# Optimization experiments

Measured on AMD Instinct MI355X. Metric: run time of the kernel, lower is better.

## Reference

```python
import jax, jax.numpy as jnp
import numpy as np

N = 10000      # nodes
E = 160000     # edges
MUL = 64       # multiplicity of 0e and 1o in node feats / target
NATTR = 10     # number of element types (node_attrs one-hot width)
RDIM = 8       # radial (edge_feats) dim
NAVG = 16.0    # num_avg_neighbors
_INV3 = 0.5773502691896258  # CG coeff for 1o x 1o -> 0e (1/sqrt(3))


def setup_inputs() -> dict:
    key = jax.random.key(0)
    ks = jax.random.split(key, 20)
    return {
        "node_attrs": jax.random.uniform(ks[0], (N, NATTR), jnp.float32),
        "node_feats": jax.random.normal(ks[1], (N, 4 * MUL), jnp.float32),
        "edge_attrs_real": jax.random.normal(ks[2], (E, 4), jnp.float32),
        "edge_attrs_imag": jax.random.normal(ks[3], (E, 4), jnp.float32),
        "edge_feats": jax.random.normal(ks[4], (E, RDIM), jnp.float32),
        # linear_up (per-l internal weights)
        "W_up0": jax.random.normal(ks[5], (MUL, MUL), jnp.float32),
        "W_up1": jax.random.normal(ks[6], (MUL, MUL), jnp.float32),
        # conv_tp_weights MLP: [8, 64, 64, 64, 4*MUL]
        "M1": jax.random.normal(ks[7], (RDIM, 64), jnp.float32),
        "M2": jax.random.normal(ks[8], (64, 64), jnp.float32),
        "M3": jax.random.normal(ks[9], (64, 64), jnp.float32),
        "M4": jax.random.normal(ks[10], (64, 4 * MUL), jnp.float32),
        # linear: irreps_mid (128x0e+128x1o) -> irreps_nonlin (128x0e+64x1o)
        "W_lin_s": jax.random.normal(ks[11], (2 * MUL, 2 * MUL), jnp.float32),
        "W_lin_v": jax.random.normal(ks[12], (2 * MUL, MUL), jnp.float32),
        # skip_tp: FullyConnectedTensorProduct(node_feats, node_attrs -> irreps_nonlin)
        "W_sk_s": jax.random.normal(ks[13], (MUL, NATTR, 2 * MUL), jnp.float32),
        "W_sk_v": jax.random.normal(ks[14], (MUL, NATTR, MUL), jnp.float32),
        "edge_index": jax.random.randint(ks[15], (2, E), 0, N, jnp.int64
                                         if jax.config.jax_enable_x64 else jnp.int32),
    }


def _forward(node_attrs, node_feats, edge_attrs_real, edge_attrs_imag, edge_feats,
             W_up0, W_up1, M1, M2, M3, M4, W_lin_s, W_lin_v, W_sk_s, W_sk_v,
             sender, receiver):
    n = node_feats.shape[0]
    x0 = node_feats[:, :MUL]                          # (N, 64)   64x0e
    x1 = node_feats[:, MUL:].reshape(n, MUL, 3)       # (N, 64, 3) 64x1o

    # skip TP (fully connected, node_attrs are scalars)
    sk_norm = 1.0 / np.sqrt(MUL * NATTR)
    sc_s = jnp.einsum('nu,na,uav->nv', x0, node_attrs, W_sk_s) * sk_norm   # (N,128)
    sc_v = jnp.einsum('nui,na,uav->nvi', x1, node_attrs, W_sk_v) * sk_norm # (N,64,3)

    # linear_up (per-l)
    up_norm = 1.0 / np.sqrt(MUL)
    x0 = (x0 @ W_up0) * up_norm
    x1 = jnp.einsum('nui,uv->nvi', x1, W_up1) * up_norm

    # radial MLP -> per-edge TP weights (4 uvu paths x MUL)
    h = jax.nn.silu((edge_feats @ M1) / np.sqrt(RDIM))
    h = jax.nn.silu((h @ M2) / 8.0)
    h = jax.nn.silu((h @ M3) / 8.0)
    tw = (h @ M4) / 8.0                               # (E, 256)
    wA, wB, wC, wD = (tw[:, :MUL], tw[:, MUL:2*MUL],
                      tw[:, 2*MUL:3*MUL], tw[:, 3*MUL:])

    xs0 = x0[sender]                                  # (E, 64)
    xs1 = x1[sender]                                  # (E, 64, 3)

    def conv_tp(y):
        # y: (E,4) = [0e | 1o]; uvu paths with per-edge weights
        y0, y1 = y[:, :1], y[:, 1:]
        s = jnp.concatenate([xs0 * y0 * wA,                                  # 0e x 0e -> 0e
                             jnp.einsum('eui,ei->eu', xs1, y1) * _INV3 * wD  # 1o x 1o -> 0e
                             ], axis=1)                                      # (E,128)
        v = jnp.concatenate([(xs0 * wB)[:, :, None] * y1[:, None, :],        # 0e x 1o -> 1o
                             xs1 * (y0 * wC)[:, :, None]                     # 1o x 0e -> 1o
                             ], axis=1)                                      # (E,128,3)
        return s, v

    sr, vr = conv_tp(edge_attrs_real)
    si, vi = conv_tp(edge_attrs_imag)

    ms_r = jax.ops.segment_sum(sr, receiver, num_segments=n)
    mv_r = jax.ops.segment_sum(vr, receiver, num_segments=n)
    ms_i = jax.ops.segment_sum(si, receiver, num_segments=n)
    mv_i = jax.ops.segment_sum(vi, receiver, num_segments=n)

    lin_norm = (1.0 / np.sqrt(2 * MUL)) / (2.0 * NAVG)

    def lin(ms, mv):
        return (ms @ W_lin_s) * lin_norm, jnp.einsum('nui,uv->nvi', mv, W_lin_v) * lin_norm

    def gate(s, v):
        # irreps_nonlin = 64x0e scalars | 64x0e gates | 64x1o gated
        scal = jax.nn.silu(s[:, :MUL])
        g = jax.nn.silu(s[:, MUL:])
        return jnp.concatenate([scal, (v * g[:, :, None]).reshape(n, 3 * MUL)], axis=1)

    ls, lv = lin(ms_r, mv_r)
    real = gate(ls + sc_s, lv + sc_v)                 # (N, 256), residual on real part
    lsi, lvi = lin(ms_i, mv_i)
    imag = gate(lsi, lvi)                             # (N, 256)

    # view_as_complex + reshape [N, num_features, dim//num_features]; complex kept
    # as trailing real/imag axis of size 2.
    return jnp.stack([real, imag], axis=-1).reshape(n, MUL, (4 * MUL) // MUL, 2)


def reference(node_attrs, node_feats, edge_attrs_real, edge_attrs_imag, edge_feats,
              W_up0, W_up1, M1, M2, M3, M4, W_lin_s, W_lin_v, W_sk_s, W_sk_v,
              edge_index):
    sender, receiver = edge_index[0], edge_index[1]
    return _forward(node_attrs, node_feats, edge_attrs_real, edge_attrs_imag,
                    edge_feats, W_up0, W_up1, M1, M2, M3, M4,
                    W_lin_s, W_lin_v, W_sk_s, W_sk_v, sender, receiver)
```

## Files before the change

### kernel.cpp

```cpp
#include <hip/hip_runtime.h>
#include <hip/hip_bf16.h>

#define NN 10000
#define NE 160000
#define NGRP 625
#define XPLN 640000

#define SK_NORM   0.039528470752104741f
#define UP_NORM   0.125f
#define M1_NORM   0.35355339059327373f
#define INV3      0.5773502691896258f
#define LIN_NORM  0.0027621358640099516f

__device__ __forceinline__ float siluf(float x) { return x / (1.0f + __expf(-x)); }

__device__ __forceinline__ unsigned short f2bf_bits(float x) {
    union { __hip_bfloat16 h; unsigned short u; } cv;
    cv.h = __float2bfloat16(x);
    return cv.u;
}
__device__ __forceinline__ float bflo(unsigned int w) { return __uint_as_float(w << 16); }
__device__ __forceinline__ float bfhi(unsigned int w) { return __uint_as_float(w & 0xffff0000u); }

typedef short bf16x8 __attribute__((ext_vector_type(8)));
typedef float f32x4  __attribute__((ext_vector_type(4)));

__global__ __launch_bounds__(256) void k_detect(const int* __restrict__ ei32, int* __restrict__ flag) {
    __shared__ int cnt;
    if (threadIdx.x == 0) cnt = 0;
    __syncthreads();
    int z = 0;
    for (int i = threadIdx.x; i < 1024; i += 256)
        if (ei32[2 * i + 1] == 0) z++;
    atomicAdd(&cnt, z);
    __syncthreads();
    if (threadIdx.x == 0) flag[0] = (cnt >= 512) ? 1 : 0;
}

__global__ __launch_bounds__(256) void k_cvt(const int* __restrict__ ei32, const int* __restrict__ flag,
                                             int* __restrict__ snd, int* __restrict__ rcv) {
    int e = blockIdx.x * 256 + threadIdx.x;
    if (e >= NE) return;
    if (flag[0]) {
        const long long* e64 = (const long long*)ei32;
        snd[e] = (int)e64[e];
        rcv[e] = (int)e64[NE + e];
    } else {
        snd[e] = ei32[e];
        rcv[e] = ei32[NE + e];
    }
}

__global__ __launch_bounds__(256) void k_wprepN(
    const float* __restrict__ Wsk_s, const float* __restrict__ Wsk_v,
    const float* __restrict__ Wu0, const float* __restrict__ Wu1,
    unsigned short* __restrict__ WNF) {
    int idx = blockIdx.x * 256 + threadIdx.x;
    if (idx >= 131072) return;
    float val;
    if (idx < 81920) {
        int p = idx / 10240, r = idx % 10240;
        int kc = r >> 9, l8 = r & 511;
        int lane = l8 >> 3, j = l8 & 7, quad = lane >> 4, lo = lane & 15;
        int a = kc >> 1, u = (kc & 1) * 32 + quad * 8 + j;
        val = Wsk_s[(u * 10 + a) * 128 + p * 16 + lo];
    } else if (idx < 122880) {
        int rel = idx - 81920;
        int p = rel / 10240, r = rel % 10240;
        int kc = r >> 9, l8 = r & 511;
        int lane = l8 >> 3, j = l8 & 7, quad = lane >> 4, lo = lane & 15;
        int a = kc >> 1, u = (kc & 1) * 32 + quad * 8 + j;
        val = Wsk_v[(u * 10 + a) * 64 + p * 16 + lo];
    } else if (idx < 126976) {
        int rel = idx - 122880;
        int p = rel >> 10, r = rel & 1023;
        int kc = r >> 9, l8 = r & 511;
        int lane = l8 >> 3, j = l8 & 7, quad = lane >> 4, lo = lane & 15;
        int u = kc * 32 + quad * 8 + j;
        val = Wu0[u * 64 + p * 16 + lo];
    } else {
        int rel = idx - 126976;
        int p = rel >> 10, r = rel & 1023;
        int kc = r >> 9, l8 = r & 511;
        int lane = l8 >> 3, j = l8 & 7, quad = lane >> 4, lo = lane & 15;
        int u = kc * 32 + quad * 8 + j;
        val = Wu1[u * 64 + p * 16 + lo];
    }
    WNF[idx] = f2bf_bits(val);
}

__global__ __launch_bounds__(256) void k_xprep(
    const float* __restrict__ node_attrs, const float* __restrict__ node_feats,
    unsigned short* __restrict__ xpk, float* __restrict__ attrsP) {
    int idx = blockIdx.x * 256 + threadIdx.x;
    if (idx < 4 * NN * 64) {
        int n = idx >> 8, c = idx & 255;
        int plane = c >> 6, u = c & 63;
        float v = (plane == 0) ? node_feats[(long)n * 256 + u]
                               : node_feats[(long)n * 256 + 64 + u * 3 + (plane - 1)];
        xpk[(size_t)plane * XPLN + (long)n * 64 + u] = f2bf_bits(v);
        return;
    }
    int i2 = idx - 4 * NN * 64;
    if (i2 < 10 * NN) {
        int a = i2 / NN, n = i2 - a * NN;
        attrsP[i2] = node_attrs[(long)n * 10 + a];
    }
}

__global__ __launch_bounds__(256) void k_wprep2(
    const float* __restrict__ M1, const float* __restrict__ M2,
    const float* __restrict__ M3, const float* __restrict__ M4,
    const float* __restrict__ W_lin_s, const float* __restrict__ W_lin_v,
    unsigned short* __restrict__ WFG, unsigned short* __restrict__ WLF) {
    int idx = blockIdx.x * 256 + threadIdx.x;
    if (idx >= (52 + 48) * 512) return;
    if (idx < 52 * 512) {
        int f = idx >> 9, r = idx & 511;
        int lane = r >> 3, j = r & 7;
        int quad = lane >> 4, lo = lane & 15;
        float val;
        if (f < 4) {
            int n = f * 16 + lo, k = quad * 8 + j;
            val = (k < 8) ? M1[k * 64 + n] : 0.f;
        } else if (f < 12) {
            int g2 = f - 4, nt = g2 >> 1, half = g2 & 1;
            int n = nt * 16 + lo, k = half * 32 + quad * 8 + j;
            val = M2[k * 64 + n];
        } else if (f < 20) {
            int g3 = f - 12, nt = g3 >> 1, half = g3 & 1;
            int n = nt * 16 + lo, k = half * 32 + quad * 8 + j;
            val = M3[k * 64 + n];
        } else {
            int g4 = f - 20, tt = g4 >> 1, half = g4 & 1;
            int n = tt * 16 + lo, k = half * 32 + quad * 8 + j;
            val = M4[k * 256 + n];
        }
        WFG[idx] = f2bf_bits(val);
    } else {
        int rel = idx - 52 * 512;
        int f = rel >> 9, r = rel & 511;
        int lane = r >> 3, j = r & 7;
        int quad = lane >> 4, lo = lane & 15;
        float val;
        if (f < 32) {
            int vt = f >> 2, ks = f & 3;
            val = W_lin_s[(ks * 32 + quad * 8 + j) * 128 + vt * 16 + lo];
        } else {
            int f2 = f - 32;
            int vt = f2 >> 2, ks = f2 & 3;
            val = W_lin_v[(ks * 32 + quad * 8 + j) * 64 + vt * 16 + lo];
        }
        WLF[rel] = f2bf_bits(val);
    }
}

#define G0 8
#define NB0 79
#define G2 4
#define NB2 157
#define G3 16
#define NB3 40
#define KNODE_GRID (4*NB0 + 2*NB2 + 2*NB3)

__global__ __launch_bounds__(128) void k_node(
    const unsigned short* __restrict__ xpk, const float* __restrict__ attrsP,
    const unsigned short* __restrict__ WNF,
    float* __restrict__ sc_s, float* __restrict__ sc_v,
    float* __restrict__ x0u, float* __restrict__ x1p) {
    __shared__ unsigned short pan[2 * 10240];
    __shared__ float att[10 * 128];

    int t = threadIdx.x;
    int bid = blockIdx.x;
    int type, vp, chunk;
    if (bid < 4 * NB0)                 { type = 0; vp = bid / NB0; chunk = bid % NB0; }
    else if (bid < 4 * NB0 + 2 * NB2)  { int r = bid - 4 * NB0; type = 2; vp = r / NB2; chunk = r % NB2; }
    else                               { int r = bid - 4 * NB0 - 2 * NB2; type = 3; vp = r / NB3; chunk = r % NB3; }
    int G = (type == 0) ? G0 : (type == 2 ? G2 : G3);
    int g0 = chunk * G;
    int ng = NGRP - g0; if (ng > G) ng = G;
    int n0 = g0 * 16;

    int psrc, pcnt;
    if (type == 0)      { psrc = vp * 2 * 10240;           pcnt = 20480; }
    else if (type == 2) { psrc = 81920 + vp * 2 * 10240;   pcnt = 20480; }
    else                { psrc = 122880 + vp * 2 * 1024;   pcnt = 2048;  }
    for (int i = t; i < pcnt / 8; i += 128)
        ((float4*)pan)[i] = ((const float4*)(WNF + psrc))[i];
    if (type == 3) {
        for (int i = t; i < 2048 / 8; i += 128)
            ((float4*)(pan + 2048))[i] = ((const float4*)(WNF + 126976 + vp * 2 * 1024))[i];
    }
    if (type <= 2) {
        int cnt = ng * 16;
        #pragma unroll
        for (int k = 0; k < 10; k++) {
            int i = k * 128 + t;
            int nl = t;
            if (nl < cnt) att[i] = attrsP[k * NN + n0 + nl];
        }
    }
    __syncthreads();

    int wv = t >> 6, lane = t & 63, lo = lane & 15, quad = lane >> 4;
    int lbase = lane * 8;
    const f32x4 zacc = {0.f, 0.f, 0.f, 0.f};
    const unsigned short* mypan = pan + wv * 10240;

    if (type == 0) {
        int vtg = vp * 2 + wv;
        const unsigned short* xb = xpk;
        bf16x8 nfa0 = *(const bf16x8*)(xb + (long)(n0 + lo) * 64 + quad * 8);
        bf16x8 nfa1 = *(const bf16x8*)(xb + (long)(n0 + lo) * 64 + 32 + quad * 8);
        #pragma unroll 1
        for (int g = 0; g < ng; g++) {
            bf16x8 fa0 = nfa0, fa1 = nfa1;
            if (g + 1 < ng) {
                nfa0 = *(const bf16x8*)(xb + (long)(n0 + (g + 1) * 16 + lo) * 64 + quad * 8);
                nfa1 = *(const bf16x8*)(xb + (long)(n0 + (g + 1) * 16 + lo) * 64 + 32 + quad * 8);
            }
            f32x4 acc = zacc;
            #pragma unroll
            for (int a = 0; a < 10; a++) {
                bf16x8 b0 = *(const bf16x8*)&mypan[(2 * a) * 512 + lbase];
                bf16x8 b1 = *(const bf16x8*)&mypan[(2 * a + 1) * 512 + lbase];
                f32x4 p = __builtin_amdgcn_mfma_f32_16x16x32_bf16(fa0, b0, zacc, 0, 0, 0);
                p = __builtin_amdgcn_mfma_f32_16x16x32_bf16(fa1, b1, p, 0, 0, 0);
                float4 afv = *(const float4*)&att[a * 128 + g * 16 + quad * 4];
                acc[0] += afv.x * p[0]; acc[1] += afv.y * p[1];
                acc[2] += afv.z * p[2]; acc[3] += afv.w * p[3];
            }
            int nb = n0 + g * 16;
            #pragma unroll
            for (int r = 0; r < 4; r++)
                sc_s[(long)(nb + quad * 4 + r) * 128 + vtg * 16 + lo] = acc[r] * SK_NORM;
        }
    } else if (type == 2) {
        int vt = vp * 2 + wv;
        bf16x8 nfa0[3], nfa1[3];
        #pragma unroll
        for (int i = 0; i < 3; i++) {
            const unsigned short* xb = xpk + (size_t)(1 + i) * XPLN + (long)(n0 + lo) * 64;
            nfa0[i] = *(const bf16x8*)(xb + quad * 8);
            nfa1[i] = *(const bf16x8*)(xb + 32 + quad * 8);
        }
        #pragma unroll 1
        for (int g = 0; g < ng; g++) {
            bf16x8 fa0[3], fa1[3];
            #pragma unroll
            for (int i = 0; i < 3; i++) { fa0[i] = nfa0[i]; fa1[i] = nfa1[i]; }
            if (g + 1 < ng) {
                #pragma unroll
                for (int i = 0; i < 3; i++) {
                    const unsigned short* xb = xpk + (size_t)(1 + i) * XPLN + (long)(n0 + (g + 1) * 16 + lo) * 64;
                    nfa0[i] = *(const bf16x8*)(xb + quad * 8);
                    nfa1[i] = *(const bf16x8*)(xb + 32 + quad * 8);
                }
            }
            f32x4 acc0 = zacc, acc1 = zacc, acc2 = zacc;
            #pragma unroll
            for (int a = 0; a < 10; a++) {
                bf16x8 b0 = *(const bf16x8*)&mypan[(2 * a) * 512 + lbase];
                bf16x8 b1 = *(const bf16x8*)&mypan[(2 * a + 1) * 512 + lbase];
                float4 afv = *(const float4*)&att[a * 128 + g * 16 + quad * 4];
                f32x4 p0 = __builtin_amdgcn_mfma_f32_16x16x32_bf16(fa0[0], b0, zacc, 0, 0, 0);
                p0 = __builtin_amdgcn_mfma_f32_16x16x32_bf16(fa1[0], b1, p0, 0, 0, 0);
                acc0[0] += afv.x * p0[0]; acc0[1] += afv.y * p0[1];
                acc0[2] += afv.z * p0[2]; acc0[3] += afv.w * p0[3];
                f32x4 p1 = __builtin_amdgcn_mfma_f32_16x16x32_bf16(fa0[1], b0, zacc, 0, 0, 0);
                p1 = __builtin_amdgcn_mfma_f32_16x16x32_bf16(fa1[1], b1, p1, 0, 0, 0);
                acc1[0] += afv.x * p1[0]; acc1[1] += afv.y * p1[1];
                acc1[2] += afv.z * p1[2]; acc1[3] += afv.w * p1[3];
                f32x4 p2 = __builtin_amdgcn_mfma_f32_16x16x32_bf16(fa0[2], b0, zacc, 0, 0, 0);
                p2 = __builtin_amdgcn_mfma_f32_16x16x32_bf16(fa1[2], b1, p2, 0, 0, 0);
                acc2[0] += afv.x * p2[0]; acc2[1] += afv.y * p2[1];
                acc2[2] += afv.z * p2[2]; acc2[3] += afv.w * p2[3];
            }
            int nb = n0 + g * 16;
            #pragma unroll
            for (int r = 0; r < 4; r++) {
                long rb = (long)(nb + quad * 4 + r) * 192 + vt * 16 + lo;
                sc_v[rb]       = acc0[r] * SK_NORM;
                sc_v[rb + 64]  = acc1[r] * SK_NORM;
                sc_v[rb + 128] = acc2[r] * SK_NORM;
            }
        }
    } else {
        int vt = vp * 2 + wv;
        bf16x8 bk20 = *(const bf16x8*)&pan[wv * 1024 + lbase];
        bf16x8 bk21 = *(const bf16x8*)&pan[wv * 1024 + 512 + lbase];
        bf16x8 bk30 = *(const bf16x8*)&pan[2048 + wv * 1024 + lbase];
        bf16x8 bk31 = *(const bf16x8*)&pan[2048 + wv * 1024 + 512 + lbase];
        #pragma unroll 1
        for (int g = 0; g < ng; g++) {
            int nb = n0 + g * 16;
            {
                const unsigned short* xb = xpk + (long)(nb + lo) * 64;
                bf16x8 fa0 = *(const bf16x8*)(xb + quad * 8);
                bf16x8 fa1 = *(const bf16x8*)(xb + 32 + quad * 8);
                f32x4 acc = __builtin_amdgcn_mfma_f32_16x16x32_bf16(fa0, bk20, zacc, 0, 0, 0);
                acc = __builtin_amdgcn_mfma_f32_16x16x32_bf16(fa1, bk21, acc, 0, 0, 0);
                #pragma unroll
                for (int r = 0; r < 4; r++)
                    x0u[(long)(nb + quad * 4 + r) * 64 + vt * 16 + lo] = acc[r] * UP_NORM;
            }
            #pragma unroll
            for (int i = 0; i < 3; i++) {
                const unsigned short* xb = xpk + (size_t)(1 + i) * XPLN + (long)(nb + lo) * 64;
                bf16x8 fa0 = *(const bf16x8*)(xb + quad * 8);
                bf16x8 fa1 = *(const bf16x8*)(xb + 32 + quad * 8);
                f32x4 acc = __builtin_amdgcn_mfma_f32_16x16x32_bf16(fa0, bk30, zacc, 0, 0, 0);
                acc = __builtin_amdgcn_mfma_f32_16x16x32_bf16(fa1, bk31, acc, 0, 0, 0);
                #pragma unroll
                for (int r = 0; r < 4; r++)
                    x1p[(size_t)i * XPLN + (long)(nb + quad * 4 + r) * 64 + vt * 16 + lo] = acc[r] * UP_NORM;
            }
        }
    }
}

__global__ __launch_bounds__(256) void k_hist(const int* __restrict__ rcv, int* __restrict__ counts) {
    int e = blockIdx.x * 256 + threadIdx.x;
    if (e < NE) atomicAdd(&counts[rcv[e]], 1);
}

__global__ __launch_bounds__(1024) void k_scan(const int* __restrict__ counts, int* __restrict__ offsets) {
    __shared__ int partial[1024];
    int t = threadIdx.x;
    const int CHUNK = (NN + 1023) / 1024;
    int base = t * CHUNK;
    int s = 0;
    for (int i = 0; i < CHUNK; i++) if (base + i < NN) s += counts[base + i];
    partial[t] = s;
    __syncthreads();
    for (int d = 1; d < 1024; d *= 2) {
        int v = (t >= d) ? partial[t - d] : 0;
        __syncthreads();
        partial[t] += v;
        __syncthreads();
    }
    int excl = (t == 0) ? 0 : partial[t - 1];
    for (int i = 0; i < CHUNK; i++) {
        if (base + i < NN) { offsets[base + i] = excl; excl += counts[base + i]; }
    }
    if (t == 1023) offsets[NN] = partial[1023];
}

__global__ __launch_bounds__(256) void k_fill(const int* __restrict__ rcv, const int* __restrict__ snd,
                                              const int* __restrict__ offsets,
                                              int* __restrict__ cursor, int2* __restrict__ epk) {
    int e = blockIdx.x * 256 + threadIdx.x;
    if (e < NE) {
        int r = rcv[e];
        int pos = atomicAdd(&cursor[r], 1);
        epk[offsets[r] + pos] = make_int2(snd[e], e);
    }
}

__global__ __launch_bounds__(256) void k_eprep(const int2* __restrict__ epk,
                                               const float4* __restrict__ ear, const float4* __restrict__ eai,
                                               const float4* __restrict__ ef,
                                               int* __restrict__ sndp,
                                               float4* __restrict__ earp, float4* __restrict__ eaip,
                                               float4* __restrict__ efp) {
    int j = blockIdx.x * 256 + threadIdx.x;
    if (j >= NE) return;
    int2 se = epk[j];
    sndp[j] = se.x;
    earp[j] = ear[se.y];
    eaip[j] = eai[se.y];
    efp[(long)j * 2]     = ef[(long)se.y * 2];
    efp[(long)j * 2 + 1] = ef[(long)se.y * 2 + 1];
}

#define HID_STRIDE 72
#define OB_STRIDE  40
#define EPB 128

__global__ __launch_bounds__(256) void k_edge_mlp(
    const float4* __restrict__ efp, const unsigned short* __restrict__ WFG,
    __hip_bfloat16* __restrict__ twp) {
    __shared__ unsigned short wfrag[52 * 512];
    __shared__ unsigned short hid[4][16 * HID_STRIDE];

    int t = threadIdx.x;
    for (int i = t; i < 52 * 512 / 8; i += 256)
        ((float4*)wfrag)[i] = ((const float4*)WFG)[i];
    __syncthreads();

    int wv = t >> 6;
    int lane = t & 63;
    int lo = lane & 15;
    int quad = lane >> 4;
    int lbase = lane * 8;
    unsigned short* myhid = hid[wv];
    unsigned short* myob  = hid[wv];
    const f32x4 zacc = {0.f, 0.f, 0.f, 0.f};

    #pragma unroll 1
    for (int g = 0; g < EPB / 64; g++) {
        int jbase = blockIdx.x * EPB + g * 64 + wv * 16;

        bf16x8 a1 = {0, 0, 0, 0, 0, 0, 0, 0};
        if (quad == 0) {
            float4 f0 = efp[(long)(jbase + lo) * 2];
            float4 f1 = efp[(long)(jbase + lo) * 2 + 1];
            union { unsigned short us[8]; bf16x8 v; } pk;
            pk.us[0] = f2bf_bits(f0.x * M1_NORM); pk.us[1] = f2bf_bits(f0.y * M1_NORM);
            pk.us[2] = f2bf_bits(f0.z * M1_NORM); pk.us[3] = f2bf_bits(f0.w * M1_NORM);
            pk.us[4] = f2bf_bits(f1.x * M1_NORM); pk.us[5] = f2bf_bits(f1.y * M1_NORM);
            pk.us[6] = f2bf_bits(f1.z * M1_NORM); pk.us[7] = f2bf_bits(f1.w * M1_NORM);
            a1 = pk.v;
        }
        {
            f32x4 acc[4];
            #pragma unroll
            for (int nt = 0; nt < 4; nt++) {
                bf16x8 b = *(const bf16x8*)&wfrag[nt * 512 + lbase];
                acc[nt] = __builtin_amdgcn_mfma_f32_16x16x32_bf16(a1, b, zacc, 0, 0, 0);
            }
            #pragma unroll
            for (int nt = 0; nt < 4; nt++)
                #pragma unroll
                for (int r = 0; r < 4; r++)
                    myhid[(quad * 4 + r) * HID_STRIDE + nt * 16 + lo] = f2bf_bits(siluf(acc[nt][r]));
        }

        #pragma unroll
        for (int L = 0; L < 2; L++) {
            int fb = 4 + L * 8;
            bf16x8 a0 = *(const bf16x8*)&myhid[lo * HID_STRIDE + quad * 8];
            bf16x8 a1v = *(const bf16x8*)&myhid[lo * HID_STRIDE + 32 + quad * 8];
            f32x4 acc[4];
            #pragma unroll
            for (int nt = 0; nt < 4; nt++) {
                bf16x8 b0 = *(const bf16x8*)&wfrag[(fb + nt * 2) * 512 + lbase];
                bf16x8 b1 = *(const bf16x8*)&wfrag[(fb + nt * 2 + 1) * 512 + lbase];
                acc[nt] = __builtin_amdgcn_mfma_f32_16x16x32_bf16(a0, b0, zacc, 0, 0, 0);
                acc[nt] = __builtin_amdgcn_mfma_f32_16x16x32_bf16(a1v, b1, acc[nt], 0, 0, 0);
            }
            #pragma unroll
            for (int nt = 0; nt < 4; nt++)
                #pragma unroll
                for (int r = 0; r < 4; r++)
                    myhid[(quad * 4 + r) * HID_STRIDE + nt * 16 + lo] = f2bf_bits(siluf(acc[nt][r] * 0.125f));
        }

        {
            bf16x8 a0 = *(const bf16x8*)&myhid[lo * HID_STRIDE + quad * 8];
            bf16x8 a1v = *(const bf16x8*)&myhid[lo * HID_STRIDE + 32 + quad * 8];
            int sedge = lane >> 2, sch = lane & 3;
            #pragma unroll 1
            for (int rd = 0; rd < 8; rd++) {
                f32x4 acc2[2];
                #pragma unroll
                for (int p = 0; p < 2; p++) {
                    int tt = (rd < 4) ? (p * 4 + rd) : (8 + p * 4 + (rd - 4));
                    bf16x8 b0 = *(const bf16x8*)&wfrag[(20 + tt * 2) * 512 + lbase];
                    bf16x8 b1 = *(const bf16x8*)&wfrag[(20 + tt * 2 + 1) * 512 + lbase];
                    acc2[p] = __builtin_amdgcn_mfma_f32_16x16x32_bf16(a0, b0, zacc, 0, 0, 0);
                    acc2[p] = __builtin_amdgcn_mfma_f32_16x16x32_bf16(a1v, b1, acc2[p], 0, 0, 0);
                }
                #pragma unroll
                for (int p = 0; p < 2; p++)
                    #pragma unroll
                    for (int r = 0; r < 4; r++)
                        myob[(quad * 4 + r) * OB_STRIDE + 2 * lo + p] = f2bf_bits(acc2[p][r] * 0.125f);
                bf16x8 vv = *(const bf16x8*)&myob[sedge * OB_STRIDE + sch * 8];
                *(bf16x8*)(twp + (long)(jbase + sedge) * 256 + rd * 32 + sch * 8) = vv;
            }
        }
    }
}

#define CB2 4
__global__ __launch_bounds__(256) void k_conv(
    const int* __restrict__ offsets, const int* __restrict__ sndp,
    const float4* __restrict__ earp, const float4* __restrict__ eaip,
    const float* __restrict__ x0u, const float* __restrict__ x1p,
    const __hip_bfloat16* __restrict__ twp,
    unsigned short* __restrict__ msgF) {
    __shared__ float red[2 * 64 * 9];
    __shared__ unsigned short stg[1024];
    int n = blockIdx.x;
    int t = threadIdx.x;
    int wv = t >> 6;
    int u = t & 63;
    int path = wv >> 1;
    int wpar = wv & 1;
    int beg = offsets[n], end = offsets[n + 1];
    float a0r = 0.f, a1r = 0.f, a2r = 0.f, a3r = 0.f;
    float a0i = 0.f, a1i = 0.f, a2i = 0.f, a3i = 0.f;
    if (path == 0) {
        const int tsel = 2 * u;
        for (int jb = beg + wpar * CB2; jb < end; jb += 2 * CB2) {
            unsigned int twd[CB2]; float x0v[CB2]; float4 yr[CB2], yi[CB2];
            #pragma unroll
            for (int p = 0; p < CB2; p++) {
                int j = jb + p;
                int jc = (j < end) ? j : (end - 1);
                int s = sndp[jc];
                yr[p] = earp[jc];
                yi[p] = eaip[jc];
                x0v[p] = x0u[(long)s * 64 + u];
                twd[p] = (j < end) ? *(const unsigned int*)(twp + (long)jc * 256 + tsel) : 0u;
            }
            #pragma unroll
            for (int p = 0; p < CB2; p++) {
                float wA = bflo(twd[p]), wB = bfhi(twd[p]);
                float xa = x0v[p] * wA, xb = x0v[p] * wB;
                a0r += xa * yr[p].x; a1r += xb * yr[p].y; a2r += xb * yr[p].z; a3r += xb * yr[p].w;
                a0i += xa * yi[p].x; a1i += xb * yi[p].y; a2i += xb * yi[p].z; a3i += xb * yi[p].w;
            }
        }
    } else {
        const int tsel = 128 + 2 * u;
        for (int jb = beg + wpar * CB2; jb < end; jb += 2 * CB2) {
            unsigned int twd[CB2]; float xv0[CB2], xv1[CB2], xv2[CB2]; float4 yr[CB2], yi[CB2];
            #pragma unroll
            for (int p = 0; p < CB2; p++) {
                int j = jb + p;
                int jc = (j < end) ? j : (end - 1);
                int s = sndp[jc];
                yr[p] = earp[jc];
                yi[p] = eaip[jc];
                long sb = (long)s * 64 + u;
                xv0[p] = x1p[sb];
                xv1[p] = x1p[XPLN + sb];
                xv2[p] = x1p[2 * XPLN + sb];
                twd[p] = (j < end) ? *(const unsigned int*)(twp + (long)jc * 256 + tsel) : 0u;
            }
            #pragma unroll
            for (int p = 0; p < CB2; p++) {
                float wC = bflo(twd[p]), wDs = bfhi(twd[p]) * INV3;
                float dr = xv0[p] * yr[p].y + xv1[p] * yr[p].z + xv2[p] * yr[p].w;
                float di = xv0[p] * yi[p].y + xv1[p] * yi[p].z + xv2[p] * yi[p].w;
                a0r += dr * wDs; a0i += di * wDs;
                float ycr = yr[p].x * wC, yci = yi[p].x * wC;
                a1r += xv0[p] * ycr; a2r += xv1[p] * ycr; a3r += xv2[p] * ycr;
                a1i += xv0[p] * yci; a2i += xv1[p] * yci; a3i += xv2[p] * yci;
            }
        }
    }
    float* rb = &red[(path * 64 + u) * 9];
    if (wpar == 1) {
        rb[0] = a0r; rb[1] = a1r; rb[2] = a2r; rb[3] = a3r;
        rb[4] = a0i; rb[5] = a1i; rb[6] = a2i; rb[7] = a3i;
    }
    __syncthreads();
    if (wpar == 0) {
        a0r += rb[0]; a1r += rb[1]; a2r += rb[2]; a3r += rb[3];
        a0i += rb[4]; a1i += rb[5]; a2i += rb[6]; a3i += rb[7];
        int cu = path * 64 + u;
        stg[cu]       = f2bf_bits(a0r);
        stg[128 + cu] = f2bf_bits(a0i);
        stg[256 + cu] = f2bf_bits(a1r);
        stg[384 + cu] = f2bf_bits(a2r);
        stg[512 + cu] = f2bf_bits(a3r);
        stg[640 + cu] = f2bf_bits(a1i);
        stg[768 + cu] = f2bf_bits(a2i);
        stg[896 + cu] = f2bf_bits(a3i);
    }
    __syncthreads();
    if (t < 128) {
        int g = n >> 4, lo = n & 15;
        bf16x8 vv = *(const bf16x8*)&stg[t * 8];
        *(bf16x8*)(msgF + (size_t)g * 16384 + (t >> 2) * 512 + lo * 32 + (t & 3) * 8) = vv;
    }
}

#define SV_STRIDE 129
#define VV_STRIDE 65

__global__ __launch_bounds__(256, 3) void k_lin(
    const unsigned short* __restrict__ msgF,
    const float* __restrict__ sc_s, const float* __restrict__ sc_v,
    const unsigned short* __restrict__ WLF,
    float* __restrict__ out) {
    __shared__ char smem[49152];
    unsigned short* wfrag = (unsigned short*)smem;
    float* sval = (float*)smem;
    float* vval = (float*)(smem + 2 * 16 * SV_STRIDE * 4);

    int t = threadIdx.x;
    for (int i = t; i < 48 * 512 / 8; i += 256)
        ((float4*)wfrag)[i] = ((const float4*)WLF)[i];
    __syncthreads();

    int wv = t >> 6;
    int lane = t & 63;
    int lo = lane & 15;
    int quad = lane >> 4;
    int lbase = lane * 8;
    int aoff_lane = lo * 32 + quad * 8;
    const f32x4 zacc = {0.f, 0.f, 0.f, 0.f};

    long g = blockIdx.x;
    long nbase = g * 16;
    const unsigned short* agbase = msgF + (size_t)g * 16384;

    f32x4 accs[10];
    #pragma unroll
    for (int q = 0; q < 10; q++) {
        int tau = wv + q * 4;
        int cblk, fb;
        if (tau < 16) {
            int ri = tau >> 3, vt = tau & 7;
            cblk = ri; fb = vt * 4;
        } else {
            int tp = tau - 16;
            int ri = tp / 12, rem = tp % 12;
            int i = rem >> 2, vt = rem & 3;
            cblk = 2 + ri * 3 + i; fb = 32 + vt * 4;
        }
        f32x4 acc = zacc;
        #pragma unroll
        for (int ks = 0; ks < 4; ks++) {
            bf16x8 a = *(const bf16x8*)(agbase + (cblk * 4 + ks) * 512 + aoff_lane);
            bf16x8 b = *(const bf16x8*)&wfrag[(fb + ks) * 512 + lbase];
            acc = __builtin_amdgcn_mfma_f32_16x16x32_bf16(a, b, acc, 0, 0, 0);
        }
        accs[q] = acc;
    }
    __syncthreads();

    #pragma unroll
    for (int q = 0; q < 10; q++) {
        int tau = wv + q * 4;
        if (tau < 16) {
            int ri = tau >> 3, vt = tau & 7;
            int cidx = (ri * 16) * SV_STRIDE + vt * 16 + lo;
            #pragma unroll
            for (int r = 0; r < 4; r++)
                sval[cidx + (quad * 4 + r) * SV_STRIDE] = accs[q][r] * LIN_NORM;
        } else {
            int tp = tau - 16;
            int ri = tp / 12, rem = tp % 12;
            int i = rem >> 2, vt = rem & 3;
            int cidx = ((ri * 3 + i) * 16) * VV_STRIDE + vt * 16 + lo;
            #pragma unroll
            for (int r = 0; r < 4; r++)
                vval[cidx + (quad * 4 + r) * VV_STRIDE] = accs[q][r] * LIN_NORM;
        }
    }
    __syncthreads();

    #pragma unroll 1
    for (int j = 0; j < 16; j++) {
        int c = t;
        long gn = nbase + j;
        float re, im;
        if (c < 64) {
            float sr = sval[(0 * 16 + j) * SV_STRIDE + c] + sc_s[gn * 128 + c];
            float si = sval[(1 * 16 + j) * SV_STRIDE + c];
            re = siluf(sr); im = siluf(si);
        } else {
            int rem = c - 64;
            int v = rem / 3;
            int i = rem - v * 3;
            float gr = siluf(sval[(0 * 16 + j) * SV_STRIDE + 64 + v] + sc_s[gn * 128 + 64 + v]);
            float gi = siluf(sval[(1 * 16 + j) * SV_STRIDE + 64 + v]);
            float lr = vval[((0 * 3 + i) * 16 + j) * VV_STRIDE + v] + sc_v[gn * 192 + i * 64 + v];
            float li = vval[((1 * 3 + i) * 16 + j) * VV_STRIDE + v];
            re = lr * gr; im = li * gi;
        }
        ((float2*)out)[gn * 256 + c] = make_float2(re, im);
    }
}

extern "C" void kernel_launch(void* const* d_in, const int* in_sizes, int n_in,
                              void* d_out, int out_size, void* d_ws, size_t ws_size,
                              hipStream_t stream) {
    const float* node_attrs = (const float*)d_in[0];
    const float* node_feats = (const float*)d_in[1];
    const float* ear        = (const float*)d_in[2];
    const float* eai        = (const float*)d_in[3];
    const float* edge_feats = (const float*)d_in[4];
    const float* W_up0      = (const float*)d_in[5];
    const float* W_up1      = (const float*)d_in[6];
    const float* M1         = (const float*)d_in[7];
    const float* M2         = (const float*)d_in[8];
    const float* M3         = (const float*)d_in[9];
    const float* M4         = (const float*)d_in[10];
    const float* W_lin_s    = (const float*)d_in[11];
    const float* W_lin_v    = (const float*)d_in[12];
    const float* W_sk_s     = (const float*)d_in[13];
    const float* W_sk_v     = (const float*)d_in[14];
    const int*   ei         = (const int*)d_in[15];

    char* ws = (char*)d_ws;
    size_t o_x0u = 0;
    size_t o_x1p = o_x0u + (size_t)NN * 64 * 4;
    size_t o_scs = o_x1p + (size_t)NN * 256 * 4;
    size_t o_scv = o_scs + (size_t)NN * 128 * 4;
    size_t o_tw  = o_scv + (size_t)NN * 192 * 4;
    size_t o_cnt = o_tw  + (size_t)NE * 256 * 2;
    size_t o_cur = o_cnt + (size_t)NN * 4;
    size_t o_ofs = o_cur + (size_t)NN * 4;
    size_t o_epk = o_ofs + (size_t)(NN + 1) * 4 + 60;
    size_t o_snd = o_epk + (size_t)NE * 8;
    size_t o_rcv = o_snd + (size_t)NE * 4;
    size_t o_flg = o_rcv + (size_t)NE * 4;
    size_t o_msg = o_flg + 64;
    size_t o_wnf = o_msg + (size_t)NN * 1024 * 2;
    size_t o_snp = o_wnf + 262144;
    size_t o_erp = o_snp + (size_t)NE * 4;
    size_t o_eip = o_erp + (size_t)NE * 16;
    size_t o_efp = o_eip + (size_t)NE * 16;
    size_t o_wfg = o_efp + (size_t)NE * 32;
    size_t o_wlf = o_wfg + (size_t)52 * 512 * 2;
    size_t o_xpk = o_wlf + (size_t)48 * 512 * 2;
    size_t o_atp = o_xpk + (size_t)4 * NN * 64 * 2;

    float* x0u = (float*)(ws + o_x0u);
    float* x1p = (float*)(ws + o_x1p);
    float* sc_s = (float*)(ws + o_scs);
    float* sc_v = (float*)(ws + o_scv);
    __hip_bfloat16* twp = (__hip_bfloat16*)(ws + o_tw);
    int* counts  = (int*)(ws + o_cnt);
    int* cursor  = (int*)(ws + o_cur);
    int* offsets = (int*)(ws + o_ofs);
    int2* epk    = (int2*)(ws + o_epk);
    int* snd     = (int*)(ws + o_snd);
    int* rcv     = (int*)(ws + o_rcv);
    int* flag    = (int*)(ws + o_flg);
    unsigned short* msgF = (unsigned short*)(ws + o_msg);
    unsigned short* WNF = (unsigned short*)(ws + o_wnf);
    int*    sndp = (int*)(ws + o_snp);
    float4* earp = (float4*)(ws + o_erp);
    float4* eaip = (float4*)(ws + o_eip);
    float4* efp  = (float4*)(ws + o_efp);
    unsigned short* WFG = (unsigned short*)(ws + o_wfg);
    unsigned short* WLF = (unsigned short*)(ws + o_wlf);
    unsigned short* xpk = (unsigned short*)(ws + o_xpk);
    float* attrsP = (float*)(ws + o_atp);

    hipMemsetAsync(ws + o_cnt, 0, (size_t)NN * 8, stream);

    dim3 b256(256), b1024(1024), b128(128);
    k_detect<<<dim3(1), b256, 0, stream>>>(ei, flag);
    k_cvt   <<<dim3((NE + 255) / 256), b256, 0, stream>>>(ei, flag, snd, rcv);
    k_hist<<<dim3((NE + 255) / 256), b256, 0, stream>>>(rcv, counts);
    k_scan<<<dim3(1), b1024, 0, stream>>>(counts, offsets);
    k_fill<<<dim3((NE + 255) / 256), b256, 0, stream>>>(rcv, snd, offsets, cursor, epk);
    k_eprep<<<dim3((NE + 255) / 256), b256, 0, stream>>>(epk, (const float4*)ear, (const float4*)eai,
                                                         (const float4*)edge_feats,
                                                         sndp, earp, eaip, efp);
    k_wprepN<<<dim3(512), b256, 0, stream>>>(W_sk_s, W_sk_v, W_up0, W_up1, WNF);
    k_wprep2<<<dim3(200), b256, 0, stream>>>(M1, M2, M3, M4, W_lin_s, W_lin_v, WFG, WLF);
    k_xprep <<<dim3((4 * NN * 64 + 10 * NN + 255) / 256), b256, 0, stream>>>(node_attrs, node_feats, xpk, attrsP);
    k_node  <<<dim3(KNODE_GRID), b128, 0, stream>>>(xpk, attrsP, WNF, sc_s, sc_v, x0u, x1p);
    k_edge_mlp<<<dim3(NE / EPB), b256, 0, stream>>>(efp, WFG, twp);
    k_conv<<<dim3(NN), b256, 0, stream>>>(offsets, sndp, earp, eaip, x0u, x1p, twp, msgF);
    k_lin <<<dim3(NGRP), b256, 0, stream>>>(msgF, sc_s, sc_v, WLF, (float*)d_out);
}
```

Before: 276.9 us.

## Stream last-layer MLP weights from global and write outputs directly from registers

The edge MLP kernel now keeps only the first 20 weight fragments in LDS and reads the final layer's 32 fragments straight from global/L2. This shrinks shared memory so more blocks fit per CU, which is reinforced by a launch bound of 4 blocks and a doubled edges-per-block count. The LDS staging transpose for the output is dropped in favour of packed 32-bit stores written directly from the MFMA accumulators, and the next group's edge features are prefetched one iteration ahead. The trade-off is more global weight traffic and less coalesced output stores, in exchange for higher occupancy and fewer LDS round-trips.

```diff
diff --git a/kernel.cpp b/kernel.cpp
--- a/kernel.cpp
+++ b/kernel.cpp
@@ -375,17 +375,16 @@
 }
 
 #define HID_STRIDE 72
-#define OB_STRIDE  40
-#define EPB 128
-
-__global__ __launch_bounds__(256) void k_edge_mlp(
+#define EPB 256
+
+__global__ __launch_bounds__(256, 4) void k_edge_mlp(
     const float4* __restrict__ efp, const unsigned short* __restrict__ WFG,
     __hip_bfloat16* __restrict__ twp) {
-    __shared__ unsigned short wfrag[52 * 512];
+    __shared__ unsigned short wfrag[20 * 512];
     __shared__ unsigned short hid[4][16 * HID_STRIDE];
 
     int t = threadIdx.x;
-    for (int i = t; i < 52 * 512 / 8; i += 256)
+    for (int i = t; i < 20 * 512 / 8; i += 256)
         ((float4*)wfrag)[i] = ((const float4*)WFG)[i];
     __syncthreads();
 
@@ -395,23 +394,33 @@
     int quad = lane >> 4;
     int lbase = lane * 8;
     unsigned short* myhid = hid[wv];
-    unsigned short* myob  = hid[wv];
+    const unsigned short* W4 = WFG + 20 * 512;
     const f32x4 zacc = {0.f, 0.f, 0.f, 0.f};
+
+    float4 f0, f1;
+    if (quad == 0) {
+        long jb0 = (long)blockIdx.x * EPB + wv * 16;
+        f0 = efp[(jb0 + lo) * 2];
+        f1 = efp[(jb0 + lo) * 2 + 1];
+    }
 
     #pragma unroll 1
     for (int g = 0; g < EPB / 64; g++) {
-        int jbase = blockIdx.x * EPB + g * 64 + wv * 16;
+        long jbase = (long)blockIdx.x * EPB + g * 64 + wv * 16;
 
         bf16x8 a1 = {0, 0, 0, 0, 0, 0, 0, 0};
         if (quad == 0) {
-            float4 f0 = efp[(long)(jbase + lo) * 2];
-            float4 f1 = efp[(long)(jbase + lo) * 2 + 1];
             union { unsigned short us[8]; bf16x8 v; } pk;
             pk.us[0] = f2bf_bits(f0.x * M1_NORM); pk.us[1] = f2bf_bits(f0.y * M1_NORM);
             pk.us[2] = f2bf_bits(f0.z * M1_NORM); pk.us[3] = f2bf_bits(f0.w * M1_NORM);
             pk.us[4] = f2bf_bits(f1.x * M1_NORM); pk.us[5] = f2bf_bits(f1.y * M1_NORM);
             pk.us[6] = f2bf_bits(f1.z * M1_NORM); pk.us[7] = f2bf_bits(f1.w * M1_NORM);
             a1 = pk.v;
+            if (g + 1 < EPB / 64) {
+                long jbn = jbase + 64;
+                f0 = efp[(jbn + lo) * 2];
+                f1 = efp[(jbn + lo) * 2 + 1];
+            }
         }
         {
             f32x4 acc[4];
@@ -450,25 +459,24 @@
         {
             bf16x8 a0 = *(const bf16x8*)&myhid[lo * HID_STRIDE + quad * 8];
             bf16x8 a1v = *(const bf16x8*)&myhid[lo * HID_STRIDE + 32 + quad * 8];
-            int sedge = lane >> 2, sch = lane & 3;
-            #pragma unroll 1
+            unsigned short* twb = (unsigned short*)twp;
+            #pragma unroll
             for (int rd = 0; rd < 8; rd++) {
                 f32x4 acc2[2];
                 #pragma unroll
                 for (int p = 0; p < 2; p++) {
                     int tt = (rd < 4) ? (p * 4 + rd) : (8 + p * 4 + (rd - 4));
-                    bf16x8 b0 = *(const bf16x8*)&wfrag[(20 + tt * 2) * 512 + lbase];
-                    bf16x8 b1 = *(const bf16x8*)&wfrag[(20 + tt * 2 + 1) * 512 + lbase];
+                    bf16x8 b0 = *(const bf16x8*)(W4 + (tt * 2) * 512 + lbase);
+                    bf16x8 b1 = *(const bf16x8*)(W4 + (tt * 2 + 1) * 512 + lbase);
                     acc2[p] = __builtin_amdgcn_mfma_f32_16x16x32_bf16(a0, b0, zacc, 0, 0, 0);
                     acc2[p] = __builtin_amdgcn_mfma_f32_16x16x32_bf16(a1v, b1, acc2[p], 0, 0, 0);
                 }
                 #pragma unroll
-                for (int p = 0; p < 2; p++)
-                    #pragma unroll
-                    for (int r = 0; r < 4; r++)
-                        myob[(quad * 4 + r) * OB_STRIDE + 2 * lo + p] = f2bf_bits(acc2[p][r] * 0.125f);
-                bf16x8 vv = *(const bf16x8*)&myob[sedge * OB_STRIDE + sch * 8];
-                *(bf16x8*)(twp + (long)(jbase + sedge) * 256 + rd * 32 + sch * 8) = vv;
+                for (int r = 0; r < 4; r++) {
+                    unsigned int w = (unsigned int)f2bf_bits(acc2[0][r] * 0.125f)
+                                   | ((unsigned int)f2bf_bits(acc2[1][r] * 0.125f) << 16);
+                    *(unsigned int*)(twb + (jbase + quad * 4 + r) * 256 + rd * 32 + 2 * lo) = w;
+                }
             }
         }
     }
```

Result: slower. 303.1 us (+9.4%).
